# Kernel optimization log

Hardware: AMD Instinct MI355X
Metric: run time of the kernel (lower is better)

The kernel has to match this reference:

```python
import jax, jax.numpy as jnp
import numpy as np

D = 64        # input_dim (also per-head dim)
H = 8         # num_heads
L = 128       # split_length (block size)
NEG = -1e9


def _causal_mask(n):
    # additive causal mask: 0 on/below diagonal, -1e9 above
    i = jnp.arange(n)
    return jnp.where(i[:, None] >= i[None, :], 0.0, NEG).astype(jnp.float32)


def setup_inputs() -> dict:
    key = jax.random.key(0)
    ks = jax.random.split(key, 11)
    B, S = 4, 8192
    s = 1.0 / np.sqrt(D)
    inp = {
        "Q": jax.random.normal(ks[0], (B, S, D), jnp.float32),
        "K": jax.random.normal(ks[1], (B, S, D), jnp.float32),
        "V": jax.random.normal(ks[2], (B, S, D), jnp.float32),
        "WQ_w": jax.random.normal(ks[3], (H * D, D), jnp.float32) * s,
        "WQ_b": jnp.zeros((H * D,), jnp.float32),
        "WK_w": jax.random.normal(ks[4], (H * D, D), jnp.float32) * s,
        "WK_b": jnp.zeros((H * D,), jnp.float32),
        "WV_w": jax.random.normal(ks[5], (H * D, D), jnp.float32) * s,
        "WV_b": jnp.zeros((H * D,), jnp.float32),
        "W_w": jax.random.normal(ks[6], (D, H * D), jnp.float32) * (1.0 / np.sqrt(H * D)),
        "W_b": jnp.zeros((D,), jnp.float32),
    }
    return inp


def reference(Q, K, V, WQ_w, WQ_b, WK_w, WK_b, WV_w, WV_b, W_w, W_b):
    B, S, _ = Q.shape
    n = S // L  # number of blocks
    scale = 1.0 / jnp.sqrt(jnp.float32(D))

    def split(x, w, b):
        y = x @ w.T + b                              # [B,S,H*D]
        y = y.reshape(B, n, L, H, D)
        return y.transpose(0, 1, 3, 2, 4)            # [B,n,H,L,D]

    rQ = split(Q, WQ_w, WQ_b)
    rK = split(K, WK_w, WK_b)
    rV = split(V, WV_w, WV_b)

    # block-local causal attention
    s_mask = _causal_mask(L)
    Si = jnp.einsum('bnhqd,bnhkd->bnhqk', rQ, rK) * scale + s_mask
    sim = jax.nn.softmax(Si, axis=-1)
    oV = jnp.einsum('bnhqk,bnhkd->bnhqd', sim, rV)   # [B,n,H,L,D]

    # pooled global attention over blocks
    pooling = oV.mean(axis=3).transpose(0, 2, 1, 3)  # [B,H,n,D]
    g_mask = _causal_mask(n)
    g_Si = jnp.einsum('bhqd,bhkd->bhqk', pooling, pooling) * scale + g_mask
    g_sim = jax.nn.softmax(g_Si, axis=-1)
    global_att = jnp.einsum('bhqk,bhkd->bhqd', g_sim, pooling)  # [B,H,n,D]
    global_att = global_att.transpose(0, 2, 1, 3)    # [B,n,H,D]

    # broadcast-add global context to every position in the block
    oV = oV + global_att[:, :, :, None, :]           # [B,n,H,L,D]

    # merge heads then output projection
    merged = oV.transpose(0, 1, 3, 2, 4).reshape(B, S, H * D)
    out = merged @ W_w.T + W_b                       # [B,S,D]
    return out
```

## Files before the change

kernel.cpp:

```cpp
#include <hip/hip_runtime.h>
#include <stdint.h>

typedef float  v4f  __attribute__((ext_vector_type(4)));
typedef __bf16 v8bf __attribute__((ext_vector_type(8)));
typedef __bf16 v4bf __attribute__((ext_vector_type(4)));
typedef unsigned short u16;

#define NEGBIG (-1.0e9f)

static __device__ __forceinline__ uint2 pack4(v4f a){
  v4bf r;
  r[0]=(__bf16)a[0]; r[1]=(__bf16)a[1]; r[2]=(__bf16)a[2]; r[3]=(__bf16)a[3];
  return __builtin_bit_cast(uint2, r);
}
static __device__ __forceinline__ v8bf pack8(float4 a, float4 b){
  v8bf r;
  r[0]=(__bf16)a.x; r[1]=(__bf16)a.y; r[2]=(__bf16)a.z; r[3]=(__bf16)a.w;
  r[4]=(__bf16)b.x; r[5]=(__bf16)b.y; r[6]=(__bf16)b.z; r[7]=(__bf16)b.w;
  return r;
}
static __device__ __forceinline__ v4f mfma16(v8bf a, v8bf b, v4f c){
  return __builtin_amdgcn_mfma_f32_16x16x32_bf16(a, b, c, 0, 0, 0);
}

static __device__ __forceinline__ void setprio_graded(int w){
  if (w >= 6)      __builtin_amdgcn_s_setprio(3);
  else if (w >= 4) __builtin_amdgcn_s_setprio(2);
  else if (w >= 2) __builtin_amdgcn_s_setprio(1);
  else             __builtin_amdgcn_s_setprio(0);
}

static __device__ __forceinline__ v8bf bfly(uint2 t0, uint2 t1, int srcA, int srcB, int hi){
  int a0 = __shfl((int)t0.x, srcA), a1 = __shfl((int)t0.y, srcA);
  int b0 = __shfl((int)t1.x, srcA), b1 = __shfl((int)t1.y, srcA);
  int a2 = __shfl((int)t0.x, srcB), a3 = __shfl((int)t0.y, srcB);
  int b2 = __shfl((int)t1.x, srcB), b3 = __shfl((int)t1.y, srcB);
  uint4 r;
  r.x = hi ? (unsigned)b0 : (unsigned)a0;
  r.y = hi ? (unsigned)b1 : (unsigned)a1;
  r.z = hi ? (unsigned)b2 : (unsigned)a2;
  r.w = hi ? (unsigned)b3 : (unsigned)a3;
  return __builtin_bit_cast(v8bf, r);
}

__global__ __launch_bounds__(256) void k_pre(
    const float* __restrict__ WQ, const float* __restrict__ WK,
    const float* __restrict__ WV, const float* __restrict__ Ww,
    u16* __restrict__ wq, u16* __restrict__ wk,
    u16* __restrict__ wv, u16* __restrict__ ww)
{
  const int seg = blockIdx.x >> 5;
  const int idx = ((blockIdx.x & 31)*256 + threadIdx.x)*4;
  const float* s = (seg==0) ? WQ : (seg==1) ? WK : (seg==2) ? WV : Ww;
  u16*       dst = (seg==0) ? wq : (seg==1) ? wk : (seg==2) ? wv : ww;
  float4 v = *(const float4*)(s + idx);
  v4f a; a[0]=v.x; a[1]=v.y; a[2]=v.z; a[3]=v.w;
  *(uint2*)(dst + idx) = pack4(a);
}

#define LDS_RK    0
#define LDS_VT    16384
#define LDS_WS    32768
#define LDS_WW    57344
#define LDS_POOL  73728
#define LDS_BIAS  77824
#define LDS_TOTAL 80896

__global__ __launch_bounds__(512, 4) void k_fused(
    const float* __restrict__ Q, const float* __restrict__ K, const float* __restrict__ V,
    const u16* __restrict__ wqbf, const u16* __restrict__ wkbf,
    const u16* __restrict__ wvbf, const u16* __restrict__ wwbf,
    const float* __restrict__ bQ, const float* __restrict__ bK, const float* __restrict__ bV,
    float* __restrict__ oVW, float* __restrict__ pool)
{
  extern __shared__ char lds[];

  const int bid = blockIdx.x;
  const int hg  = bid >> 8;
  const int tile = bid & 255;
  const int b = tile >> 6, nb = tile & 63;
  const int rowbase = tile * 128;
  const int tid = threadIdx.x;
  const int w = tid >> 6, l = tid & 63;
  const int l15 = l & 15, g = l >> 4;
  const int swz = (l15 & 7) << 4;
  const int srcA = ((l >> 4) & 1) * 32 + l15;
  const int srcB = srcA + 16;
  const int hi_  = l >> 5;
  const float scale = 0.125f;

  auto STAGE = [&](int hn, int wbuf){
    #pragma unroll
    for (int i = 0; i < 4; ++i){
      const int obase = w*4096 + i*1024;
      const int m   = obase >> 13;
      const int row = ((obase & 8191) >> 7) + (l >> 3);
      const int sc  = (l & 7) << 4;
      const char* src;
      int dst;
      if (m == 3){
        src = (const char*)wwbf + row*1024 + hn*128 + (sc ^ ((row & 7) << 4));
        dst = LDS_WW + wbuf*8192 + (obase - 24576);
      } else {
        const u16* basep = (m == 0) ? wqbf : (m == 1) ? wkbf : wvbf;
        src = (const char*)basep + hn*8192 + row*128 + (sc ^ ((row & 7) << 4));
        dst = LDS_WS + obase;
      }
      __builtin_amdgcn_global_load_lds(
          (const __attribute__((address_space(1))) unsigned int*)src,
          (__attribute__((address_space(3))) unsigned int*)(lds + dst),
          16, 0, 0);
    }
  };

  STAGE(hg*4, 0);

  if (tid < 192){
    const int arr = tid >> 6;
    const int idx = (tid & 63) * 4;
    const float* srcb = (arr==0) ? bQ : (arr==1) ? bK : bV;
    *(float4*)(lds + LDS_BIAS + arr*1024 + idx*4) = *(const float4*)(srcb + hg*256 + idx);
  }

  const int xrow = rowbase + w*16 + l15;
  v8bf xq[2], xk[2], xv[2];
  #pragma unroll
  for (int ks = 0; ks < 2; ++ks){
    const float* qp = Q + xrow*64 + ks*32 + g*8;
    const float* kp = K + xrow*64 + ks*32 + g*8;
    const float* vp = V + xrow*64 + ks*32 + g*8;
    xq[ks] = pack8(*(const float4*)qp, *(const float4*)(qp+4));
    xk[ks] = pack8(*(const float4*)kp, *(const float4*)(kp+4));
    xv[ks] = pack8(*(const float4*)vp, *(const float4*)(vp+4));
  }

  __syncthreads();

  v4f acc_out[4];
  #pragma unroll
  for (int mt = 0; mt < 4; ++mt){ v4f z = {0.f,0.f,0.f,0.f}; acc_out[mt] = z; }

  const int q = w*16 + l15;
  const float* bql = (const float*)(lds + LDS_BIAS);
  const float* bkl = bql + 256;
  const float* bvl = bql + 512;

  for (int hi = 0; hi < 4; ++hi){
    const int h  = hg*4 + hi;
    char* wsb = lds + LDS_WS;

    v4f aq[4], ak[4];
    #pragma unroll
    for (int mt = 0; mt < 4; ++mt){
      float4 b4 = *(const float4*)(bql + hi*64 + mt*16 + g*4);
      aq[mt][0]=b4.x; aq[mt][1]=b4.y; aq[mt][2]=b4.z; aq[mt][3]=b4.w;
      float4 c4 = *(const float4*)(bkl + hi*64 + mt*16 + g*4);
      ak[mt][0]=c4.x; ak[mt][1]=c4.y; ak[mt][2]=c4.z; ak[mt][3]=c4.w;
    }
    #pragma unroll
    for (int ks = 0; ks < 2; ++ks){
      #pragma unroll
      for (int mt = 0; mt < 4; ++mt){
        v8bf wqf = *(const v8bf*)(wsb + (mt*16 + l15)*128 + ((ks*64 + g*16) ^ swz));
        aq[mt] = mfma16(wqf, xq[ks], aq[mt]);
      }
      #pragma unroll
      for (int mt = 0; mt < 4; ++mt){
        v8bf wkf = *(const v8bf*)(wsb + 8192 + (mt*16 + l15)*128 + ((ks*64 + g*16) ^ swz));
        ak[mt] = mfma16(wkf, xk[ks], ak[mt]);
      }
    }
    uint2 pq[4];
    #pragma unroll
    for (int mt = 0; mt < 4; ++mt) pq[mt] = pack4(aq[mt]);
    v8bf qf0 = bfly(pq[0], pq[1], srcA, srcB, hi_);
    v8bf qf1 = bfly(pq[2], pq[3], srcA, srcB, hi_);
    #pragma unroll
    for (int mt = 0; mt < 4; ++mt)
      *(uint2*)(lds + LDS_RK + (w*16 + l15)*128 + ((mt*32 + g*8) ^ swz)) = pack4(ak[mt]);

    {
      v4f av[4];
      #pragma unroll
      for (int nt = 0; nt < 4; ++nt){
        float bs = bvl[hi*64 + nt*16 + l15];
        av[nt][0]=bs; av[nt][1]=bs; av[nt][2]=bs; av[nt][3]=bs;
      }
      #pragma unroll
      for (int ks = 0; ks < 2; ++ks)
        #pragma unroll
        for (int nt = 0; nt < 4; ++nt){
          v8bf wvf = *(const v8bf*)(wsb + 16384 + (nt*16 + l15)*128 + ((ks*64 + g*16) ^ swz));
          av[nt] = mfma16(xv[ks], wvf, av[nt]);
        }
      #pragma unroll
      for (int nt = 0; nt < 4; ++nt)
        *(uint2*)(lds + LDS_VT + (nt*16 + l15)*256 + ((w*32 + g*8) ^ swz)) = pack4(av[nt]);
    }

    __syncthreads();

    if (hi < 3) STAGE(h+1, (hi+1)&1);

    if (hi > 0 && tid < 64){
      const float* pr = (const float*)(lds + LDS_POOL + ((hi-1)&1)*2048);
      float s_ = 0.f;
      #pragma unroll
      for (int p = 0; p < 8; ++p) s_ += pr[p*64 + tid];
      pool[(b*8 + h-1)*4096 + nb*64 + tid] = s_ * (1.0f/128.0f);
    }

    setprio_graded(w);

    float sum = 0.f;
    uint2 pp[8];
    #pragma unroll
    for (int mt = 0; mt < 8; ++mt){
      if (mt > w){ uint2 z; z.x = 0u; z.y = 0u; pp[mt] = z; continue; }
      v4f s4 = {0.f,0.f,0.f,0.f};
      s4 = mfma16(*(const v8bf*)(lds + LDS_RK + (mt*16 + l15)*128 + ((0*64 + g*16) ^ swz)), qf0, s4);
      s4 = mfma16(*(const v8bf*)(lds + LDS_RK + (mt*16 + l15)*128 + ((1*64 + g*16) ^ swz)), qf1, s4);
      v4f e4;
      #pragma unroll
      for (int r = 0; r < 4; ++r){
        const int key = mt*16 + g*4 + r;
        float v_ = (key <= q) ? s4[r]*scale : NEGBIG;
        float p = __expf(v_);
        e4[r] = p;
        sum += p;
      }
      pp[mt] = pack4(e4);
    }
    sum += __shfl_xor(sum, 16);
    sum += __shfl_xor(sum, 32);
    const float inv = 1.0f / sum;

    v4f oa[4];
    #pragma unroll
    for (int mt = 0; mt < 4; ++mt){ v4f z = {0.f,0.f,0.f,0.f}; oa[mt] = z; }
    const int WKn = (w >> 1) + 1;
    #pragma unroll
    for (int ks = 0; ks < 4; ++ks){
      if (ks >= WKn) continue;
      v8bf pf = bfly(pp[2*ks], pp[2*ks+1], srcA, srcB, hi_);
      #pragma unroll
      for (int mt = 0; mt < 4; ++mt){
        v8bf vf = *(const v8bf*)(lds + LDS_VT + (mt*16 + l15)*256 + ((ks*64 + g*16) ^ swz));
        oa[mt] = mfma16(vf, pf, oa[mt]);
      }
    }

    #pragma unroll
    for (int mt = 0; mt < 4; ++mt){
      oa[mt][0]*=inv; oa[mt][1]*=inv; oa[mt][2]*=inv; oa[mt][3]*=inv;
    }

    {
      float* prd = (float*)(lds + LDS_POOL + (hi&1)*2048);
      #pragma unroll
      for (int mt = 0; mt < 4; ++mt){
        v4f v = oa[mt];
        #pragma unroll
        for (int s_ = 1; s_ < 16; s_ <<= 1){
          v[0] += __shfl_xor(v[0], s_);
          v[1] += __shfl_xor(v[1], s_);
          v[2] += __shfl_xor(v[2], s_);
          v[3] += __shfl_xor(v[3], s_);
        }
        if (l15 == 0)
          *(float4*)(prd + w*64 + mt*16 + g*4) = make_float4(v[0], v[1], v[2], v[3]);
      }
    }

    uint2 po[4];
    #pragma unroll
    for (int mt = 0; mt < 4; ++mt) po[mt] = pack4(oa[mt]);
    v8bf of0 = bfly(po[0], po[1], srcA, srcB, hi_);
    v8bf of1 = bfly(po[2], po[3], srcA, srcB, hi_);
    {
      const char* wwb = lds + LDS_WW + (hi&1)*8192;
      #pragma unroll
      for (int ks = 0; ks < 2; ++ks){
        v8bf off = ks ? of1 : of0;
        #pragma unroll
        for (int mt = 0; mt < 4; ++mt){
          v8bf wf = *(const v8bf*)(wwb + (mt*16 + l15)*128 + ((ks*64 + g*16) ^ swz));
          acc_out[mt] = mfma16(wf, off, acc_out[mt]);
        }
      }
    }

    __builtin_amdgcn_s_setprio(0);
    __syncthreads();
  }

  if (tid < 64){
    const float* pr = (const float*)(lds + LDS_POOL + (3&1)*2048);
    float s_ = 0.f;
    #pragma unroll
    for (int p = 0; p < 8; ++p) s_ += pr[p*64 + tid];
    pool[(b*8 + hg*4 + 3)*4096 + nb*64 + tid] = s_ * (1.0f/128.0f);
  }

  #pragma unroll
  for (int mt = 0; mt < 4; ++mt){
    float4 o;
    o.x = acc_out[mt][0]; o.y = acc_out[mt][1];
    o.z = acc_out[mt][2]; o.w = acc_out[mt][3];
    *(float4*)(oVW + hg*2097152 + (rowbase + w*16 + l15)*64 + mt*16 + g*4) = o;
  }
}

__global__ __launch_bounds__(512) void k_final(
    const float* __restrict__ oVW, const float* __restrict__ Ww, const float* __restrict__ Wb,
    const float* __restrict__ pool, float* __restrict__ out)
{
  __shared__ float prow[8][64];
  __shared__ float grow[8][64];
  __shared__ float gred[8][64];
  __shared__ float gadd[64];

  const int bid = blockIdx.x;
  const int b = bid >> 6, nb = bid & 63;
  const int rowbase = bid * 128;
  const int tid = threadIdx.x;
  const int w = tid >> 6, l = tid & 63;

  const float* pb = pool + (b*8 + w)*4096;

  float dot = 0.f;
  #pragma unroll
  for (int dd = 0; dd < 16; ++dd){
    float4 t  = *(const float4*)(pb + l*64  + dd*4);
    float4 qv = *(const float4*)(pb + nb*64 + dd*4);
    dot += t.x*qv.x + t.y*qv.y + t.z*qv.z + t.w*qv.w;
  }
  float sv = (l <= nb) ? dot*0.125f : NEGBIG;
  float mx = sv;
  #pragma unroll
  for (int s = 1; s < 64; s <<= 1) mx = fmaxf(mx, __shfl_xor(mx, s));
  float p = __expf(sv - mx);
  float sum = p;
  #pragma unroll
  for (int s = 1; s < 64; s <<= 1) sum += __shfl_xor(sum, s);
  prow[w][l] = p / sum;

  {
    float a = 0.f;
    for (int k = 0; k <= nb; ++k)
      a += prow[w][k] * pb[k*64 + l];
    grow[w][l] = a;
  }

  {
    const float* wr = Ww + l*512 + w*64;
    float c = 0.f;
    #pragma unroll
    for (int dd = 0; dd < 16; ++dd){
      float4 g4 = *(const float4*)(&grow[w][dd*4]);
      float4 w4 = *(const float4*)(wr + dd*4);
      c += g4.x*w4.x + g4.y*w4.y + g4.z*w4.z + g4.w*w4.w;
    }
    gred[w][l] = c;
  }
  __syncthreads();
  if (tid < 64){
    float s = Wb[tid];
    #pragma unroll
    for (int ph = 0; ph < 8; ++ph) s += gred[ph][tid];
    gadd[tid] = s;
  }
  __syncthreads();

  const int c4 = (tid & 15) * 4;
  float4 ga = *(const float4*)(&gadd[c4]);
  #pragma unroll
  for (int it = 0; it < 4; ++it){
    const int row = it*32 + (tid >> 4);
    const int idx = (rowbase + row)*64 + c4;
    float4 v0 = *(const float4*)(oVW + idx);
    float4 v1 = *(const float4*)(oVW + 2097152 + idx);
    float4 o;
    o.x = v0.x + v1.x + ga.x; o.y = v0.y + v1.y + ga.y;
    o.z = v0.z + v1.z + ga.z; o.w = v0.w + v1.w + ga.w;
    *(float4*)(out + idx) = o;
  }
}


extern "C" void kernel_launch(void* const* d_in, const int* in_sizes, int n_in,
                              void* d_out, int out_size, void* d_ws, size_t ws_size,
                              hipStream_t stream) {
  const float* Q   = (const float*)d_in[0];
  const float* K   = (const float*)d_in[1];
  const float* V   = (const float*)d_in[2];
  const float* WQw = (const float*)d_in[3];
  const float* WQb = (const float*)d_in[4];
  const float* WKw = (const float*)d_in[5];
  const float* WKb = (const float*)d_in[6];
  const float* WVw = (const float*)d_in[7];
  const float* WVb = (const float*)d_in[8];
  const float* Ww  = (const float*)d_in[9];
  const float* Wb  = (const float*)d_in[10];

  char* ws = (char*)d_ws;
  float* oVW  = (float*)(ws + 0);
  float* pool = (float*)(ws + 16777216);
  u16*   wqbf = (u16*)(ws + 17825792);
  u16*   wkbf = (u16*)(ws + 17891328);
  u16*   wvbf = (u16*)(ws + 17956864);
  u16*   wwbf = (u16*)(ws + 18022400);

  float* outp = (float*)d_out;

  k_pre<<<128, 256, 0, stream>>>(WQw, WKw, WVw, Ww, wqbf, wkbf, wvbf, wwbf);
  k_fused<<<512, 512, LDS_TOTAL, stream>>>(Q, K, V, wqbf, wkbf, wvbf, wwbf,
                                           WQb, WKb, WVb, oVW, pool);
  k_final<<<256, 512, 0, stream>>>(oVW, Ww, Wb, pool, outp);
}
```

Before: 79.66 us.

## Read output-projection weights from global and transpose fragments via per-wave LDS scratch

Stops staging the output-projection weight slice into double-buffered LDS and instead loads the bf16 fragments for each head directly from global memory inside the MFMA loop. The freed LDS region becomes a per-wave scratch area. The Q and O accumulator fragments are now transposed by writing them there and reading them back, replacing the cross-lane butterfly shuffles. This cuts staging work per head and the shuffle instructions. In exchange it adds LDS round trips and global-load latency on the critical path of the output accumulation.

```diff
diff --git a/kernel.cpp b/kernel.cpp
--- a/kernel.cpp
+++ b/kernel.cpp
@@ -61,7 +61,7 @@
 #define LDS_RK    0
 #define LDS_VT    16384
 #define LDS_WS    32768
-#define LDS_WW    57344
+#define LDS_QS    57344
 #define LDS_POOL  73728
 #define LDS_BIAS  77824
 #define LDS_TOTAL 80896
@@ -88,32 +88,25 @@
   const int srcB = srcA + 16;
   const int hi_  = l >> 5;
   const float scale = 0.125f;
-
-  auto STAGE = [&](int hn, int wbuf){
-    #pragma unroll
-    for (int i = 0; i < 4; ++i){
-      const int obase = w*4096 + i*1024;
+  char* const qsc = lds + LDS_QS + w*2048 + l15*128;
+
+  auto STAGE = [&](int hn){
+    #pragma unroll
+    for (int i = 0; i < 3; ++i){
+      const int obase = w*3072 + i*1024;
       const int m   = obase >> 13;
       const int row = ((obase & 8191) >> 7) + (l >> 3);
       const int sc  = (l & 7) << 4;
-      const char* src;
-      int dst;
-      if (m == 3){
-        src = (const char*)wwbf + row*1024 + hn*128 + (sc ^ ((row & 7) << 4));
-        dst = LDS_WW + wbuf*8192 + (obase - 24576);
-      } else {
-        const u16* basep = (m == 0) ? wqbf : (m == 1) ? wkbf : wvbf;
-        src = (const char*)basep + hn*8192 + row*128 + (sc ^ ((row & 7) << 4));
-        dst = LDS_WS + obase;
-      }
+      const u16* basep = (m == 0) ? wqbf : (m == 1) ? wkbf : wvbf;
+      const char* src = (const char*)basep + hn*8192 + row*128 + (sc ^ ((row & 7) << 4));
       __builtin_amdgcn_global_load_lds(
           (const __attribute__((address_space(1))) unsigned int*)src,
-          (__attribute__((address_space(3))) unsigned int*)(lds + dst),
+          (__attribute__((address_space(3))) unsigned int*)(lds + LDS_WS + obase),
           16, 0, 0);
     }
   };
 
-  STAGE(hg*4, 0);
+  STAGE(hg*4);
 
   if (tid < 192){
     const int arr = tid >> 6;
@@ -147,6 +140,7 @@
 
   for (int hi = 0; hi < 4; ++hi){
     const int h  = hg*4 + hi;
+    const int hb = h*64;
     char* wsb = lds + LDS_WS;
 
     v4f aq[4], ak[4];
@@ -170,11 +164,11 @@
         ak[mt] = mfma16(wkf, xk[ks], ak[mt]);
       }
     }
-    uint2 pq[4];
-    #pragma unroll
-    for (int mt = 0; mt < 4; ++mt) pq[mt] = pack4(aq[mt]);
-    v8bf qf0 = bfly(pq[0], pq[1], srcA, srcB, hi_);
-    v8bf qf1 = bfly(pq[2], pq[3], srcA, srcB, hi_);
+    #pragma unroll
+    for (int mt = 0; mt < 4; ++mt)
+      *(uint2*)(qsc + ((mt*32 + g*8) ^ swz)) = pack4(aq[mt]);
+    v8bf qf0 = *(const v8bf*)(qsc + ((g*16) ^ swz));
+    v8bf qf1 = *(const v8bf*)(qsc + ((64 + g*16) ^ swz));
     #pragma unroll
     for (int mt = 0; mt < 4; ++mt)
       *(uint2*)(lds + LDS_RK + (w*16 + l15)*128 + ((mt*32 + g*8) ^ swz)) = pack4(ak[mt]);
@@ -200,7 +194,7 @@
 
     __syncthreads();
 
-    if (hi < 3) STAGE(h+1, (hi+1)&1);
+    if (hi < 3) STAGE(h+1);
 
     if (hi > 0 && tid < 64){
       const float* pr = (const float*)(lds + LDS_POOL + ((hi-1)&1)*2048);
@@ -272,21 +266,18 @@
       }
     }
 
-    uint2 po[4];
-    #pragma unroll
-    for (int mt = 0; mt < 4; ++mt) po[mt] = pack4(oa[mt]);
-    v8bf of0 = bfly(po[0], po[1], srcA, srcB, hi_);
-    v8bf of1 = bfly(po[2], po[3], srcA, srcB, hi_);
-    {
-      const char* wwb = lds + LDS_WW + (hi&1)*8192;
-      #pragma unroll
-      for (int ks = 0; ks < 2; ++ks){
-        v8bf off = ks ? of1 : of0;
-        #pragma unroll
-        for (int mt = 0; mt < 4; ++mt){
-          v8bf wf = *(const v8bf*)(wwb + (mt*16 + l15)*128 + ((ks*64 + g*16) ^ swz));
-          acc_out[mt] = mfma16(wf, off, acc_out[mt]);
-        }
+    #pragma unroll
+    for (int mt = 0; mt < 4; ++mt)
+      *(uint2*)(qsc + ((mt*32 + g*8) ^ swz)) = pack4(oa[mt]);
+    v8bf of0 = *(const v8bf*)(qsc + ((g*16) ^ swz));
+    v8bf of1 = *(const v8bf*)(qsc + ((64 + g*16) ^ swz));
+    #pragma unroll
+    for (int ks = 0; ks < 2; ++ks){
+      v8bf off = ks ? of1 : of0;
+      #pragma unroll
+      for (int mt = 0; mt < 4; ++mt){
+        v8bf wf = *(const v8bf*)(wwbf + (mt*16 + l15)*512 + hb + ks*32 + g*8);
+        acc_out[mt] = mfma16(wf, off, acc_out[mt]);
       }
     }
 
```

Measured after the change: 76.91 us. -3.4%, faster.
